# Kernel tuning notes

Hardware: AMD Instinct MI355X
Metric: run time of the kernel (lower is better)

## Reference

```python
import jax, jax.numpy as jnp
import numpy as np

S, H, D, NL = 3, 64, 12, 2  # scales, hidden, input_dim, layers
B, L = 512, 512
EPS = 1e-5


def _layernorm(x, g, b):
    m = jnp.mean(x, axis=-1, keepdims=True)
    v = jnp.var(x, axis=-1, keepdims=True)
    return (x - m) * jax.lax.rsqrt(v + EPS) * g + b


def _cell(x_t, h, c, gw, gb, mi_w, mi_b, mo_w, mo_b, w1, b1, w2, b2, lag, lab, log, lob):
    # fused 4-gate linear: [B, in+H] @ [in+H, 4H]
    gates = jnp.concatenate([x_t, h], axis=-1) @ gw + gb
    f, i, g, o = jnp.split(gates, 4, axis=-1)
    c_new = jax.nn.sigmoid(f) * c + jax.nn.sigmoid(i) * jnp.tanh(g)
    h_t = jax.nn.sigmoid(o) * jnp.tanh(c_new)
    # MultiheadAttention with seq_len=1: softmax over one key == 1,
    # so attn_out = out_proj(v_proj(h_t)) exactly (q/k contribute nothing).
    v = h_t @ mi_w[:, 2 * H:] + mi_b[2 * H:]
    a = v @ mo_w + mo_b
    a = jax.nn.gelu(a @ w1 + b1, approximate=False) @ w2 + b2
    a = _layernorm(a, lag, lab)
    return _layernorm(a + h, log, lob), c_new


def _run_xlstm(xi, gw0, gb0, gw1, gb1, mi_w, mi_b, mo_w, mo_b,
               w1, b1, w2, b2, lag, lab, log, lob, rw0, rb0, rw1, rb1):
    # xi: [B, L, D] -> outputs [B, L, H]; 2-layer unidirectional xLSTM (eval: dropout=identity)
    Bb = xi.shape[0]
    z = jnp.zeros((Bb, H), xi.dtype)

    def step(carry, x_t):
        h0, c0, h1, c1 = carry
        h0, c0 = _cell(x_t, h0, c0, gw0, gb0, mi_w[0], mi_b[0], mo_w[0], mo_b[0],
                       w1[0], b1[0], w2[0], b2[0], lag[0], lab[0], log[0], lob[0])
        inp = h0 + x_t @ rw0 + rb0
        h1, c1 = _cell(inp, h1, c1, gw1, gb1, mi_w[1], mi_b[1], mo_w[1], mo_b[1],
                       w1[1], b1[1], w2[1], b2[1], lag[1], lab[1], log[1], lob[1])
        out = h1 + inp @ rw1 + rb1
        return (h0, c0, h1, c1), out

    _, ys = jax.lax.scan(step, (z, z, z, z), jnp.swapaxes(xi, 0, 1))
    return jnp.swapaxes(ys, 0, 1)


def _upsample_linear(xi, out_len):
    # F.interpolate(mode='linear', align_corners=False) on [B, Li, D] time axis
    Li = xi.shape[1]
    if Li == out_len:
        return xi
    sc = Li / out_len
    src = jnp.maximum((jnp.arange(out_len, dtype=jnp.float32) + 0.5) * sc - 0.5, 0.0)
    i0 = jnp.clip(jnp.floor(src).astype(jnp.int32), 0, Li - 1)
    i1 = jnp.minimum(i0 + 1, Li - 1)
    w = (src - i0.astype(jnp.float32))[None, :, None]
    return xi[:, i0] * (1.0 - w) + xi[:, i1] * w


def _forward(x, gw0, gb0, gw1, gb1, mi_w, mi_b, mo_w, mo_b, w1, b1, w2, b2,
             lag, lab, log, lob, rw0, rb0, rw1, rb1, attn_w):
    Ls = x.shape[1]
    ups = []
    for i in (1, 2, 3):
        start = Ls - Ls // i
        ups.append(_upsample_linear(x[:, start:, :], Ls))
    # bug-faithful ordering from source: xlstm[i] consumes upsampled_outputs[i-1]
    xs = jnp.stack([ups[2], ups[0], ups[1]], axis=0)  # [S, B, L, D]
    outs = jax.vmap(_run_xlstm)(xs, gw0, gb0, gw1, gb1, mi_w, mi_b, mo_w, mo_b,
                                w1, b1, w2, b2, lag, lab, log, lob,
                                rw0, rb0, rw1, rb1)      # [S, B, L, H]
    merged = jnp.moveaxis(outs, 0, 1)                    # [B, S, L, H]
    weights = jax.nn.softmax(merged @ attn_w, axis=1)    # softmax over scale dim
    return jnp.sum(merged * weights[..., None], axis=1)  # [B, L, H]


def setup_inputs() -> dict:
    key = jax.random.key(0)
    ks = iter(jax.random.split(key, 32))
    w = lambda *sh: jax.random.normal(next(ks), sh, jnp.float32) * 0.02
    IN0, IN1 = D + H, 2 * H
    return {
        'x': jax.random.normal(next(ks), (B, L, D), jnp.float32),
        'gw0': w(S, IN0, 4 * H), 'gb0': jnp.zeros((S, 4 * H)),
        'gw1': w(S, IN1, 4 * H), 'gb1': jnp.zeros((S, 4 * H)),
        'mi_w': w(S, NL, H, 3 * H), 'mi_b': jnp.zeros((S, NL, 3 * H)),
        'mo_w': w(S, NL, H, H), 'mo_b': jnp.zeros((S, NL, H)),
        'w1': w(S, NL, H, 2 * H), 'b1': jnp.zeros((S, NL, 2 * H)),
        'w2': w(S, NL, 2 * H, H), 'b2': jnp.zeros((S, NL, H)),
        'lag': jnp.ones((S, NL, H)), 'lab': jnp.zeros((S, NL, H)),
        'log': jnp.ones((S, NL, H)), 'lob': jnp.zeros((S, NL, H)),
        'rw0': w(S, D, H), 'rb0': jnp.zeros((S, H)),
        'rw1': w(S, H, H), 'rb1': jnp.zeros((S, H)),
        'attn_w': w(H),
    }


def reference(x, gw0, gb0, gw1, gb1, mi_w, mi_b, mo_w, mo_b, w1, b1, w2, b2,
              lag, lab, log, lob, rw0, rb0, rw1, rb1, attn_w):
    return _forward(x, gw0, gb0, gw1, gb1, mi_w, mi_b, mo_w, mo_b, w1, b1, w2, b2,
                    lag, lab, log, lob, rw0, rb0, rw1, rb1, attn_w)
```

## Files before the change

### kernel.cpp

```cpp
#include <hip/hip_runtime.h>
#include <hip/hip_bf16.h>
#include <math.h>

#define Sn 3
#define Hn 64
#define Dn 12
#define Bn 512
#define Ln 512
#define BC 4
#define IN0 76
#define NIN 22
#define CT 32
#define NCHUNK (Ln / CT)
#define P2OFF 0
#define P1OFF 384
#define GROFF 768
#define CBOFF 1026
#define MEGABLK 1538

#define NINP ((size_t)3 * Bn * CT * 64)
#define NG1R ((size_t)3 * Bn * CT * 320)
#define NMERG ((size_t)3 * Bn * CT * 64)

using bf16 = __hip_bfloat16;
typedef _Float16 h2 __attribute__((ext_vector_type(2)));
typedef _Float16 h4 __attribute__((ext_vector_type(4)));
typedef _Float16 h8t __attribute__((ext_vector_type(8)));
typedef int i2v __attribute__((ext_vector_type(2)));

__device__ __forceinline__ float u2f(unsigned short x) {
    return __uint_as_float(((unsigned int)x) << 16);
}
__device__ __forceinline__ unsigned short f2u(float f) {
    bf16 h = __float2bfloat16(f);
    unsigned short u;
    __builtin_memcpy(&u, &h, 2);
    return u;
}

__device__ __forceinline__ float ex2(float x) {
#if __has_builtin(__builtin_amdgcn_exp2f)
    return __builtin_amdgcn_exp2f(x);
#else
    return exp2f(x);
#endif
}
__device__ __forceinline__ float frcp(float x) {
#if __has_builtin(__builtin_amdgcn_rcpf)
    return __builtin_amdgcn_rcpf(x);
#else
    return 1.0f / x;
#endif
}
__device__ __forceinline__ float sigm(float x) {
    return frcp(1.0f + ex2(-1.44269504f * x));
}
__device__ __forceinline__ float tanhfast(float x) {
    return 1.0f - 2.0f * frcp(1.0f + ex2(2.88539008f * x));
}
__device__ __forceinline__ float gelu_ex(float x) { return 0.5f * x * (1.0f + erff(x * 0.70710678118654752f)); }

__device__ __forceinline__ float fdot2f(h2 a, h2 b, float c) {
#if __has_builtin(__builtin_amdgcn_fdot2)
    return __builtin_amdgcn_fdot2(a, b, c, false);
#else
    return fmaf((float)a.x, (float)b.x, fmaf((float)a.y, (float)b.y, c));
#endif
}
__device__ __forceinline__ h2 cvt2(float x, float y) {
    h2 r; r.x = (_Float16)x; r.y = (_Float16)y; return r;
}
__device__ __forceinline__ h2 mk2(_Float16 a, _Float16 b) {
    h2 r; r.x = a; r.y = b; return r;
}
__device__ __forceinline__ void unpack8(h8t v, h2* out) {
    out[0] = __builtin_shufflevector(v, v, 0, 1);
    out[1] = __builtin_shufflevector(v, v, 2, 3);
    out[2] = __builtin_shufflevector(v, v, 4, 5);
    out[3] = __builtin_shufflevector(v, v, 6, 7);
}

template <int CTRL>
__device__ __forceinline__ float qp(float v) {
    return __int_as_float(__builtin_amdgcn_update_dpp(0, __float_as_int(v), CTRL, 0xF, 0xF, true));
}
__device__ __forceinline__ float qsum(float v) {
    v += qp<0xB1>(v);
    v += qp<0x4E>(v);
    return v;
}
__device__ __forceinline__ float osum(float v) {
    v = qsum(v);
    v += qp<0x141>(v);
    return v;
}
__device__ __forceinline__ float xadd16(float v) {
#if __has_builtin(__builtin_amdgcn_permlane16_swap)
    i2v r = __builtin_amdgcn_permlane16_swap(__float_as_int(v), __float_as_int(v), false, false);
    return __int_as_float(r.x) + __int_as_float(r.y);
#else
    return v + __int_as_float(__builtin_amdgcn_ds_swizzle(__float_as_int(v), 0x401F));
#endif
}
__device__ __forceinline__ float xadd32(float v) {
#if __has_builtin(__builtin_amdgcn_permlane32_swap)
    i2v r = __builtin_amdgcn_permlane32_swap(__float_as_int(v), __float_as_int(v), false, false);
    return __int_as_float(r.x) + __int_as_float(r.y);
#else
    return v + __shfl_xor(v, 32, 64);
#endif
}
__device__ __forceinline__ float redsum64(float v) {
    v += qp<0xB1>(v);
    v += qp<0x4E>(v);
    v += qp<0x141>(v);
    v += qp<0x140>(v);
    v = xadd16(v);
    v = xadd32(v);
    return v;
}

__global__ __launch_bounds__(256) void detect_kernel(const unsigned short* __restrict__ xr,
                                                     int* __restrict__ flag) {
    __shared__ int sh[4];
    int tid = threadIdx.x;
    int cnt = 0;
    for (int i = tid; i < 2048; i += 256) {
        unsigned e = (xr[i] >> 7) & 0xFF;
        if (e >= 110 && e <= 133) cnt++;
    }
    for (int o = 32; o > 0; o >>= 1) cnt += __shfl_xor(cnt, o, 64);
    if ((tid & 63) == 0) sh[tid >> 6] = cnt;
    __syncthreads();
    if (tid == 0) {
        int tot = sh[0] + sh[1] + sh[2] + sh[3];
        *flag = (tot < 1640) ? 1 : 0;
    }
}

struct ConvArgs {
    const void* src[NIN];
    unsigned dstOff[NIN];
    unsigned n[NIN];
    unsigned blockStart[NIN + 1];
};

__global__ __launch_bounds__(256) void convert_kernel(ConvArgs a, float* __restrict__ dst,
                                                      const int* __restrict__ flag) {
    int bid = blockIdx.x;
    int i = 0;
    while (i < NIN - 1 && bid >= (int)a.blockStart[i + 1]) i++;
    unsigned lb = (unsigned)bid - a.blockStart[i];
    unsigned base = lb * 2048 + threadIdx.x;
    unsigned n = a.n[i];
    float* d = dst + a.dstOff[i];
    bool isf32 = (*flag != 0);
    const float* sf = (const float*)a.src[i];
    const unsigned short* su = (const unsigned short*)a.src[i];
#pragma unroll
    for (int e = 0; e < 8; e++) {
        unsigned idx = base + e * 256;
        if (idx < n) d[idx] = isf32 ? sf[idx] : u2f(su[idx]);
    }
}

__global__ __launch_bounds__(256) void fuse_kernel(
    const float* __restrict__ mi_w, const float* __restrict__ mi_b,
    const float* __restrict__ mo_w, const float* __restrict__ mo_b,
    const float* __restrict__ w1, const float* __restrict__ b1,
    float* __restrict__ M1out, float* __restrict__ bias1out) {
    int sl = blockIdx.x;
    __shared__ float T[64][64];
    __shared__ float bT[64];
    const float* Mv = mi_w + sl * 64 * 192;
    const float* Mo = mo_w + sl * 64 * 64;
    for (int idx = threadIdx.x; idx < 64 * 64; idx += 256) {
        int k = idx >> 6, n = idx & 63;
        float acc = 0.f;
        for (int j = 0; j < 64; j++) acc += Mv[k * 192 + 128 + j] * Mo[j * 64 + n];
        T[k][n] = acc;
    }
    for (int n = threadIdx.x; n < 64; n += 256) {
        float acc = mo_b[sl * 64 + n];
        for (int j = 0; j < 64; j++) acc += mi_b[sl * 192 + 128 + j] * Mo[j * 64 + n];
        bT[n] = acc;
    }
    __syncthreads();
    const float* W1 = w1 + sl * 64 * 128;
    for (int idx = threadIdx.x; idx < 64 * 128; idx += 256) {
        int k = idx >> 7, m = idx & 127;
        float acc = 0.f;
        for (int n = 0; n < 64; n++) acc += T[k][n] * W1[n * 128 + m];
        M1out[sl * 64 * 128 + idx] = acc;
    }
    for (int m = threadIdx.x; m < 128; m += 256) {
        float acc = b1[sl * 128 + m];
        for (int n = 0; n < 64; n++) acc += bT[n] * W1[n * 128 + m];
        bias1out[sl * 128 + m] = acc;
    }
}

__global__ __launch_bounds__(256) void perm_kernel(
    const float* __restrict__ gw1, const float* __restrict__ gb1,
    const float* __restrict__ rw1,
    h2* __restrict__ gw1p16, float* __restrict__ gb1p,
    h2* __restrict__ rw1p16) {
    int s = blockIdx.x;
    int tid = threadIdx.x;
    const float* G = gw1 + (size_t)s * 128 * 256;
    for (int idx = tid; idx < 32 * 256; idx += 256) {
        int k2 = idx >> 8, p = idx & 255;
        int c = (p & 3) * 64 + ((p >> 6) << 4) + ((p >> 2) & 15);
        gw1p16[((size_t)s * 32 + k2) * 256 + p] =
            cvt2(G[(2 * k2) * 256 + c], G[(2 * k2 + 1) * 256 + c]);
    }
    for (int p = tid; p < 256; p += 256) {
        int c = (p & 3) * 64 + ((p >> 6) << 4) + ((p >> 2) & 15);
        gb1p[s * 256 + p] = gb1[s * 256 + c];
    }
    const float* R = rw1 + (size_t)s * 64 * 64;
    for (int idx = tid; idx < 32 * 64; idx += 256) {
        int k2 = idx >> 6, c = idx & 63;
        rw1p16[((size_t)s * 32 + k2) * 64 + c] =
            cvt2(R[(2 * k2) * 64 + c], R[(2 * k2 + 1) * 64 + c]);
    }
}

__device__ __forceinline__ void pass1_body(
    int bid,
    const float* __restrict__ x, const float* __restrict__ gw0,
    const float* __restrict__ gb0,
    const float* __restrict__ M1g, const float* __restrict__ bias1g,
    const float* __restrict__ w2g, const float* __restrict__ b2g,
    const float* __restrict__ lag, const float* __restrict__ lab,
    const float* __restrict__ log_, const float* __restrict__ lob,
    const float* __restrict__ rw0, const float* __restrict__ rb0,
    float* __restrict__ gstate, _Float16* __restrict__ inp_w, int t0) {
    const int tid = threadIdx.x;
    const int sIdx = bid >> 7;
    const int gbase = (bid & 127) * BC;
    const int W = tid >> 6, lane = tid & 63;
    const int q = lane >> 2, ks = lane & 3;
    const int oct = lane >> 3, ks8 = lane & 7;
    const int j = W * 16 + q;
    const int cM = W * 32 + q * 2;
    const int uD = W * 16 + oct * 2;

    const int Li = (sIdx == 0) ? 170 : (sIdx == 1 ? 512 : 256);
    const int st = (sIdx == 0) ? 342 : (sIdx == 1 ? 0 : 256);
    const float sc = (float)Li / 512.0f;

    __shared__ float s_x[2][BC][12];
    __shared__ __align__(16) _Float16 s_h16[BC][72];
    __shared__ __align__(16) _Float16 s_ht16[BC][72];
    __shared__ __align__(16) _Float16 s_z16[BC][136];
    __shared__ float s_t2[BC][64];
    __shared__ float s_rw0[768];

    __builtin_amdgcn_s_setprio(1);

    const float* gw0s = gw0 + sIdx * IN0 * 256;
    float wx[12];
    h2 wg16[4][8], wm16[2][8], ww16[2][8];
#pragma unroll
    for (int g = 0; g < 4; g++)
#pragma unroll
        for (int d = 0; d < 3; d++) wx[g * 3 + d] = gw0s[(ks * 3 + d) * 256 + j + 64 * g];
#pragma unroll
    for (int g = 0; g < 4; g++)
#pragma unroll
        for (int kk = 0; kk < 8; kk++)
            wg16[g][kk] = cvt2(gw0s[(12 + ks * 16 + 2 * kk) * 256 + j + 64 * g],
                               gw0s[(12 + ks * 16 + 2 * kk + 1) * 256 + j + 64 * g]);
    const float* M1s = M1g + (sIdx * 2 + 0) * 8192;
#pragma unroll
    for (int cc = 0; cc < 2; cc++)
#pragma unroll
        for (int kk = 0; kk < 8; kk++)
            wm16[cc][kk] = cvt2(M1s[(ks * 16 + 2 * kk) * 128 + cM + cc],
                                M1s[(ks * 16 + 2 * kk + 1) * 128 + cM + cc]);
    const float* w2s = w2g + (sIdx * 2 + 0) * 8192;
#pragma unroll
    for (int cc = 0; cc < 2; cc++)
#pragma unroll
        for (int kk = 0; kk < 8; kk++)
            ww16[cc][kk] = cvt2(w2s[(ks8 * 16 + 2 * kk) * 64 + uD + cc],
                                w2s[(ks8 * 16 + 2 * kk + 1) * 64 + uD + cc]);

    float h_gb[4];
#pragma unroll
    for (int g = 0; g < 4; g++) h_gb[g] = gb0[sIdx * 256 + j + 64 * g];
    float h_b1[2] = {bias1g[(sIdx * 2 + 0) * 128 + cM], bias1g[(sIdx * 2 + 0) * 128 + cM + 1]};
    float h_b2[2] = {b2g[(sIdx * 2 + 0) * 64 + uD], b2g[(sIdx * 2 + 0) * 64 + uD + 1]};
    int ei = (sIdx * 2 + 0) * 64 + lane;
    float eLag = lag[ei], eLab = lab[ei], eLog = log_[ei], eLob = lob[ei];
    float eRb0 = rb0[sIdx * 64 + lane];

    for (int i = tid; i < 768; i += 256) s_rw0[i] = rw0[sIdx * 768 + i];
    {
        int b = tid >> 6, jj = tid & 63;
        float hv = (t0 == 0) ? 0.f : gstate[((size_t)(sIdx * Bn + gbase + b)) * 256 + jj];
        s_h16[b][jj] = (_Float16)hv;
    }
    float cS = (t0 == 0) ? 0.f
                         : gstate[((size_t)(sIdx * Bn + gbase + ks)) * 256 + 64 + j];
    if (tid < BC * 12) {
        int b = tid / 12, d = tid % 12;
        float srcp = fmaxf((t0 + 0.5f) * sc - 0.5f, 0.f);
        int i0 = (int)floorf(srcp); if (i0 > Li - 1) i0 = Li - 1;
        int i1 = i0 + 1; if (i1 > Li - 1) i1 = Li - 1;
        float w = srcp - (float)i0;
        int gb = gbase + b;
        s_x[0][b][d] = x[(gb * Ln + st + i0) * 12 + d] * (1.0f - w) + x[(gb * Ln + st + i1) * 12 + d] * w;
    }
    __syncthreads();

    for (int tt = 0; tt < CT; tt++) {
        const int sl = tt & 1;
        float myF = 0, myI = 0, myG = 0, myO = 0;
#pragma unroll
        for (int b = 0; b < BC; b++) {
            const h8t* hp = (const h8t*)&s_h16[b][ks * 16];
            h8t hv0 = hp[0], hv1 = hp[1];
            h2 hk[8];
            unpack8(hv0, hk); unpack8(hv1, hk + 4);
            float x0 = s_x[sl][b][ks * 3], x1 = s_x[sl][b][ks * 3 + 1], x2 = s_x[sl][b][ks * 3 + 2];
            float acc[4];
#pragma unroll
            for (int g = 0; g < 4; g++) {
                float s0 = (ks == 0) ? h_gb[g] : 0.f;
                acc[g] = fmaf(wx[g * 3], x0, fmaf(wx[g * 3 + 1], x1, fmaf(wx[g * 3 + 2], x2, s0)));
            }
#pragma unroll
            for (int kk = 0; kk < 8; kk++) {
#pragma unroll
                for (int g = 0; g < 4; g++)
                    acc[g] = fdot2f(wg16[g][kk], hk[kk], acc[g]);
            }
            float a0 = qsum(acc[0]);
            float a1 = qsum(acc[1]);
            float a2 = qsum(acc[2]);
            float a3 = qsum(acc[3]);
            if (ks == b) { myF = a0; myI = a1; myG = a2; myO = a3; }
        }
        {
            float cn = sigm(myF) * cS + sigm(myI) * tanhfast(myG);
            cS = cn;
            s_ht16[ks][j] = (_Float16)(sigm(myO) * tanhfast(cn));
        }
        __syncthreads();
        float z0 = 0, z1 = 0;
#pragma unroll
        for (int b = 0; b < BC; b++) {
            const h8t* hp = (const h8t*)&s_ht16[b][ks * 16];
            h8t hv0 = hp[0], hv1 = hp[1];
            h2 hk[8];
            unpack8(hv0, hk); unpack8(hv1, hk + 4);
            float acc0 = (ks == 0) ? h_b1[0] : 0.f;
            float acc1 = (ks == 0) ? h_b1[1] : 0.f;
#pragma unroll
            for (int kk = 0; kk < 8; kk++) {
                acc0 = fdot2f(wm16[0][kk], hk[kk], acc0);
                acc1 = fdot2f(wm16[1][kk], hk[kk], acc1);
            }
            float a0 = qsum(acc0);
            float a1 = qsum(acc1);
            if (ks == b) { z0 = a0; z1 = a1; }
        }
        *(h2*)&s_z16[ks][cM] = cvt2(gelu_ex(z0), gelu_ex(z1));
        __syncthreads();
#pragma unroll
        for (int b = 0; b < BC; b++) {
            const h8t* zp = (const h8t*)&s_z16[b][ks8 * 16];
            h8t zv0 = zp[0], zv1 = zp[1];
            h2 zk[8];
            unpack8(zv0, zk); unpack8(zv1, zk + 4);
            float acc0 = (ks8 == 0) ? h_b2[0] : 0.f;
            float acc1 = (ks8 == 0) ? h_b2[1] : 0.f;
#pragma unroll
            for (int kk = 0; kk < 8; kk++) {
                acc0 = fdot2f(ww16[0][kk], zk[kk], acc0);
                acc1 = fdot2f(ww16[1][kk], zk[kk], acc1);
            }
            float a0 = osum(acc0);
            float a1 = osum(acc1);
            if (ks8 == b) { s_t2[b][uD] = a0; s_t2[b][uD + 1] = a1; }
        }
        __syncthreads();
        {
            const int bb = W;
            float v = s_t2[bb][lane];
            float m = redsum64(v) * (1.0f / 64.0f);
            float var = redsum64(v * v) * (1.0f / 64.0f) - m * m;
            float rs = rsqrtf(fmaxf(var, 0.0f) + 1e-5f);
            float a = (v - m) * rs * eLag + eLab;
            float hOld = (float)s_h16[bb][lane];
            float y = a + hOld;
            float m2 = redsum64(y) * (1.0f / 64.0f);
            float var2 = redsum64(y * y) * (1.0f / 64.0f) - m2 * m2;
            float rs2 = rsqrtf(fmaxf(var2, 0.0f) + 1e-5f);
            float h0n = (y - m2) * rs2 * eLog + eLob;
            s_h16[bb][lane] = (_Float16)h0n;
            float p = h0n + eRb0;
#pragma unroll
            for (int d = 0; d < 12; d++)
                p = fmaf(s_x[sl][bb][d], s_rw0[d * 64 + lane], p);
            inp_w[(((size_t)(sIdx * Bn + gbase + bb)) * CT + tt) * 64 + lane] = (_Float16)p;
            if (tt + 1 < CT && lane < 12) {
                int d = lane;
                int t = t0 + tt + 1;
                float srcp = fmaxf((t + 0.5f) * sc - 0.5f, 0.f);
                int i0 = (int)floorf(srcp); if (i0 > Li - 1) i0 = Li - 1;
                int i1 = i0 + 1; if (i1 > Li - 1) i1 = Li - 1;
                float w = srcp - (float)i0;
                int gb = gbase + bb;
                s_x[sl ^ 1][bb][d] = x[(gb * Ln + st + i0) * 12 + d] * (1.0f - w) +
                                     x[(gb * Ln + st + i1) * 12 + d] * w;
            }
        }
        __syncthreads();
    }
    {
        int b = tid >> 6, jj = tid & 63;
        gstate[((size_t)(sIdx * Bn + gbase + b)) * 256 + jj] = (float)s_h16[b][jj];
    }
    gstate[((size_t)(sIdx * Bn + gbase + ks)) * 256 + 64 + j] = cS;
}

__device__ __forceinline__ void pass2_body(
    int bid,
    const float* __restrict__ gw1,
    const float* __restrict__ M1g, const float* __restrict__ bias1g,
    const float* __restrict__ w2g, const float* __restrict__ b2g,
    const float* __restrict__ lag, const float* __restrict__ lab,
    const float* __restrict__ log_, const float* __restrict__ lob,
    const _Float16* __restrict__ G1Rr, float* __restrict__ gstate,
    unsigned short* __restrict__ merged_w, int t0) {
    const int tid = threadIdx.x;
    const int sIdx = bid >> 7;
    const int gbase = (bid & 127) * BC;
    const int W = tid >> 6, lane = tid & 63;
    const int q = lane >> 2, ks = lane & 3;
    const int oct = lane >> 3, ks8 = lane & 7;
    const int j = W * 16 + q;
    const int cM = W * 32 + q * 2;
    const int uD = W * 16 + oct * 2;

    __shared__ __align__(16) _Float16 p2_h16[BC][72];
    __shared__ __align__(16) _Float16 p2_ht16[BC][72];
    __shared__ __align__(16) _Float16 p2_z16[BC][136];
    __shared__ float p2_t2[BC][64];

    __builtin_amdgcn_s_setprio(1);

    const float* gw1s = gw1 + (size_t)sIdx * 128 * 256;
    h2 wg16[4][8], wm16[2][8], ww16[2][8];
#pragma unroll
    for (int g = 0; g < 4; g++)
#pragma unroll
        for (int kk = 0; kk < 8; kk++)
            wg16[g][kk] = cvt2(gw1s[(64 + ks * 16 + 2 * kk) * 256 + j + 64 * g],
                               gw1s[(64 + ks * 16 + 2 * kk + 1) * 256 + j + 64 * g]);
    const float* M1s = M1g + (sIdx * 2 + 1) * 8192;
#pragma unroll
    for (int cc = 0; cc < 2; cc++)
#pragma unroll
        for (int kk = 0; kk < 8; kk++)
            wm16[cc][kk] = cvt2(M1s[(ks * 16 + 2 * kk) * 128 + cM + cc],
                                M1s[(ks * 16 + 2 * kk + 1) * 128 + cM + cc]);
    const float* w2s = w2g + (sIdx * 2 + 1) * 8192;
#pragma unroll
    for (int cc = 0; cc < 2; cc++)
#pragma unroll
        for (int kk = 0; kk < 8; kk++)
            ww16[cc][kk] = cvt2(w2s[(ks8 * 16 + 2 * kk) * 64 + uD + cc],
                                w2s[(ks8 * 16 + 2 * kk + 1) * 64 + uD + cc]);

    float h_b1[2] = {bias1g[(sIdx * 2 + 1) * 128 + cM], bias1g[(sIdx * 2 + 1) * 128 + cM + 1]};
    float h_b2[2] = {b2g[(sIdx * 2 + 1) * 64 + uD], b2g[(sIdx * 2 + 1) * 64 + uD + 1]};
    int ei = (sIdx * 2 + 1) * 64 + lane;
    float eLag = lag[ei], eLab = lab[ei], eLog = log_[ei], eLob = lob[ei];

    {
        int b = tid >> 6, jj = tid & 63;
        float hv = (t0 == 0) ? 0.f : gstate[((size_t)(sIdx * Bn + gbase + b)) * 256 + 128 + jj];
        p2_h16[b][jj] = (_Float16)hv;
    }
    float cS = (t0 == 0) ? 0.f
                         : gstate[((size_t)(sIdx * Bn + gbase + ks)) * 256 + 192 + j];
    __syncthreads();

    const size_t rowBase = ((size_t)(sIdx * Bn + gbase)) * CT;
    const int pOff = W * 64 + lane;

    float g1rv[BC], rv;
#pragma unroll
    for (int b = 0; b < BC; b++)
        g1rv[b] = (float)G1Rr[(rowBase + (size_t)b * CT) * 320 + pOff];
    rv = (float)G1Rr[(rowBase + (size_t)W * CT) * 320 + 256 + lane];

    for (int tt = 0; tt < CT; tt++) {
        float myF = 0, myI = 0, myG = 0, myO = 0;
#pragma unroll
        for (int b = 0; b < BC; b++) {
            const h8t* hp = (const h8t*)&p2_h16[b][ks * 16];
            h8t hv0 = hp[0], hv1 = hp[1];
            h2 hk[8];
            unpack8(hv0, hk); unpack8(hv1, hk + 4);
            float acc[4];
#pragma unroll
            for (int g = 0; g < 4; g++) acc[g] = (ks == g) ? g1rv[b] : 0.f;
#pragma unroll
            for (int kk = 0; kk < 8; kk++) {
#pragma unroll
                for (int g = 0; g < 4; g++)
                    acc[g] = fdot2f(wg16[g][kk], hk[kk], acc[g]);
            }
            float a0 = qsum(acc[0]);
            float a1 = qsum(acc[1]);
            float a2 = qsum(acc[2]);
            float a3 = qsum(acc[3]);
            if (ks == b) { myF = a0; myI = a1; myG = a2; myO = a3; }
        }
        {
            float cn = sigm(myF) * cS + sigm(myI) * tanhfast(myG);
            cS = cn;
            p2_ht16[ks][j] = (_Float16)(sigm(myO) * tanhfast(cn));
        }
        float g1rn[BC], rn;
        if (tt + 1 < CT) {
#pragma unroll
            for (int b = 0; b < BC; b++)
                g1rn[b] = (float)G1Rr[(rowBase + (size_t)b * CT + tt + 1) * 320 + pOff];
            rn = (float)G1Rr[(rowBase + (size_t)W * CT + tt + 1) * 320 + 256 + lane];
        } else {
#pragma unroll
            for (int b = 0; b < BC; b++) g1rn[b] = 0.f;
            rn = 0.f;
        }
        __syncthreads();
        float z0 = 0, z1 = 0;
#pragma unroll
        for (int b = 0; b < BC; b++) {
            const h8t* hp = (const h8t*)&p2_ht16[b][ks * 16];
            h8t hv0 = hp[0], hv1 = hp[1];
            h2 hk[8];
            unpack8(hv0, hk); unpack8(hv1, hk + 4);
            float acc0 = (ks == 0) ? h_b1[0] : 0.f;
            float acc1 = (ks == 0) ? h_b1[1] : 0.f;
#pragma unroll
            for (int kk = 0; kk < 8; kk++) {
                acc0 = fdot2f(wm16[0][kk], hk[kk], acc0);
                acc1 = fdot2f(wm16[1][kk], hk[kk], acc1);
            }
            float a0 = qsum(acc0);
            float a1 = qsum(acc1);
            if (ks == b) { z0 = a0; z1 = a1; }
        }
        *(h2*)&p2_z16[ks][cM] = cvt2(gelu_ex(z0), gelu_ex(z1));
        __syncthreads();
#pragma unroll
        for (int b = 0; b < BC; b++) {
            const h8t* zp = (const h8t*)&p2_z16[b][ks8 * 16];
            h8t zv0 = zp[0], zv1 = zp[1];
            h2 zk[8];
            unpack8(zv0, zk); unpack8(zv1, zk + 4);
            float acc0 = (ks8 == 0) ? h_b2[0] : 0.f;
            float acc1 = (ks8 == 0) ? h_b2[1] : 0.f;
#pragma unroll
            for (int kk = 0; kk < 8; kk++) {
                acc0 = fdot2f(ww16[0][kk], zk[kk], acc0);
                acc1 = fdot2f(ww16[1][kk], zk[kk], acc1);
            }
            float a0 = osum(acc0);
            float a1 = osum(acc1);
            if (ks8 == b) { p2_t2[b][uD] = a0; p2_t2[b][uD + 1] = a1; }
        }
        __syncthreads();
        {
            const int bb = W;
            float v = p2_t2[bb][lane];
            float m = redsum64(v) * (1.0f / 64.0f);
            float var = redsum64(v * v) * (1.0f / 64.0f) - m * m;
            float rs = rsqrtf(fmaxf(var, 0.0f) + 1e-5f);
            float a = (v - m) * rs * eLag + eLab;
            float hOld = (float)p2_h16[bb][lane];
            float y = a + hOld;
            float m2 = redsum64(y) * (1.0f / 64.0f);
            float var2 = redsum64(y * y) * (1.0f / 64.0f) - m2 * m2;
            float rs2 = rsqrtf(fmaxf(var2, 0.0f) + 1e-5f);
            float h1n = (y - m2) * rs2 * eLog + eLob;
            p2_h16[bb][lane] = (_Float16)h1n;
            merged_w[(((size_t)(sIdx * Bn + gbase + bb)) * CT + tt) * 64 + lane] = f2u(h1n + rv);
        }
        __syncthreads();
#pragma unroll
        for (int b = 0; b < BC; b++) g1rv[b] = g1rn[b];
        rv = rn;
    }
    {
        int b = tid >> 6, jj = tid & 63;
        gstate[((size_t)(sIdx * Bn + gbase + b)) * 256 + 128 + jj] = (float)p2_h16[b][jj];
    }
    gstate[((size_t)(sIdx * Bn + gbase + ks)) * 256 + 192 + j] = cS;
}

__device__ __forceinline__ void g1r_body(
    int bid,
    const h2* __restrict__ gw1p16, const float* __restrict__ gb1p,
    const h2* __restrict__ rw1p16, const float* __restrict__ rb1,
    const _Float16* __restrict__ inp_r, _Float16* __restrict__ G1Rw) {
    const int tid = threadIdx.x;
    const int s = bid / 86;
    const int bb = bid % 86;
    __shared__ __align__(16) h2 s_in2[32][36];

    const int c4 = tid & 63, rg = tid >> 6;
    float4 bias = *(const float4*)(gb1p + s * 256 + c4 * 4);
    float rbias = rb1[s * 64 + c4];
    const h2* Wg = gw1p16 + (size_t)s * 32 * 256;
    const h2* Wr = rw1p16 + (size_t)s * 32 * 64;

    const size_t sRow = (size_t)s * Bn * CT;
    for (int tile = 0; tile < 6; tile++) {
        int tIdx = bb * 6 + tile;
        if (tIdx >= 512) break;
        int r0 = tIdx * 32;
        __syncthreads();
        for (int i = tid; i < 512; i += 256) {
            int r = i >> 4, kq = i & 15;
            h4 v = *(const h4*)(inp_r + (sRow + r0 + r) * 64 + kq * 4);
            s_in2[kq * 2 + 0][r] = mk2(v.x, v.y);
            s_in2[kq * 2 + 1][r] = mk2(v.z, v.w);
        }
        __syncthreads();
        float acc[8][4], accR[8];
#pragma unroll
        for (int r = 0; r < 8; r++) {
            acc[r][0] = bias.x; acc[r][1] = bias.y; acc[r][2] = bias.z; acc[r][3] = bias.w;
            accR[r] = rbias;
        }
#pragma unroll 4
        for (int k2 = 0; k2 < 32; k2++) {
            h8t wv = *(const h8t*)(Wg + (size_t)k2 * 256 + c4 * 4);
            h2 wp[4]; unpack8(wv, wp);
            h2 wR = Wr[k2 * 64 + c4];
            const h8t* ip = (const h8t*)&s_in2[k2][rg * 8];
            h8t iv0 = ip[0], iv1 = ip[1];
            h2 in2[8]; unpack8(iv0, in2); unpack8(iv1, in2 + 4);
#pragma unroll
            for (int r = 0; r < 8; r++) {
                acc[r][0] = fdot2f(in2[r], wp[0], acc[r][0]);
                acc[r][1] = fdot2f(in2[r], wp[1], acc[r][1]);
                acc[r][2] = fdot2f(in2[r], wp[2], acc[r][2]);
                acc[r][3] = fdot2f(in2[r], wp[3], acc[r][3]);
                accR[r] = fdot2f(in2[r], wR, accR[r]);
            }
        }
#pragma unroll
        for (int r = 0; r < 8; r++) {
            size_t row = sRow + r0 + rg * 8 + r;
            h4 o;
            o.x = (_Float16)acc[r][0]; o.y = (_Float16)acc[r][1];
            o.z = (_Float16)acc[r][2]; o.w = (_Float16)acc[r][3];
            *(h4*)(G1Rw + row * 320 + c4 * 4) = o;
            G1Rw[row * 320 + 256 + c4] = (_Float16)accR[r];
        }
    }
}

__device__ __forceinline__ void combine_body(
    int bid,
    const unsigned short* __restrict__ merged_r,
    const float* __restrict__ attn_w,
    void* __restrict__ outv, const int* __restrict__ flag, int t0) {
    int W = threadIdx.x >> 6, lane = threadIdx.x & 63;
    float aw = attn_w[lane];
    size_t stride = (size_t)Bn * CT * 64;
    int isf = *flag;
#pragma unroll
    for (int r = 0; r < 8; r++) {
        int wid = (bid * 4 + W) * 8 + r;
        int b = wid >> 5, tt = wid & 31;
        size_t base = (((size_t)b) * CT + tt) * 64 + lane;
        float m0 = u2f(merged_r[base]);
        float m1 = u2f(merged_r[base + stride]);
        float m2 = u2f(merged_r[base + 2 * stride]);
        float e0 = redsum64(m0 * aw);
        float e1 = redsum64(m1 * aw);
        float e2 = redsum64(m2 * aw);
        float mx = fmaxf(e0, fmaxf(e1, e2));
        float x0 = expf(e0 - mx), x1 = expf(e1 - mx), x2 = expf(e2 - mx);
        float inv = 1.0f / (x0 + x1 + x2);
        float val = (x0 * m0 + x1 * m1 + x2 * m2) * inv;
        size_t ob = (((size_t)b) * Ln + t0 + tt) * 64 + lane;
        if (isf) ((float*)outv)[ob] = val;
        else ((unsigned short*)outv)[ob] = f2u(val);
    }
}

__global__ __launch_bounds__(256) __attribute__((amdgpu_waves_per_eu(2, 5)))
void mega_kernel(
    const float* __restrict__ x, const float* __restrict__ gw0,
    const float* __restrict__ gb0, const float* __restrict__ gw1,
    const h2* __restrict__ gw1p16, const float* __restrict__ gb1p,
    const h2* __restrict__ rw1p16,
    const float* __restrict__ M1g, const float* __restrict__ bias1g,
    const float* __restrict__ w2g, const float* __restrict__ b2g,
    const float* __restrict__ lag, const float* __restrict__ lab,
    const float* __restrict__ log_, const float* __restrict__ lob,
    const float* __restrict__ rw0, const float* __restrict__ rb0,
    const float* __restrict__ rb1,
    float* __restrict__ gstate,
    _Float16* __restrict__ inpB, _Float16* __restrict__ G1RB,
    unsigned short* __restrict__ mergedB,
    const float* __restrict__ attn_w, void* __restrict__ outv,
    const int* __restrict__ flag,
    int c_p1, int c_g1r, int c_p2, int c_comb) {
    int bid = blockIdx.x;
    if (bid < P1OFF) {
        if (c_p2 >= 0) {
            const _Float16* g1r_r = G1RB + (size_t)(c_p2 & 1) * NG1R;
            unsigned short* merged_w = mergedB + (size_t)(c_p2 & 1) * NMERG;
            pass2_body(bid, gw1, M1g, bias1g, w2g, b2g, lag, lab, log_, lob,
                       g1r_r, gstate, merged_w, c_p2 * CT);
        }
    } else if (bid < GROFF) {
        if (c_p1 >= 0) {
            _Float16* inp_w = inpB + (size_t)(c_p1 & 1) * NINP;
            pass1_body(bid - P1OFF, x, gw0, gb0, M1g, bias1g, w2g, b2g,
                       lag, lab, log_, lob, rw0, rb0, gstate, inp_w, c_p1 * CT);
        }
    } else if (bid < CBOFF) {
        if (c_g1r >= 0) {
            const _Float16* inp_r = inpB + (size_t)(c_g1r & 1) * NINP;
            _Float16* g1r_w = G1RB + (size_t)(c_g1r & 1) * NG1R;
            g1r_body(bid - GROFF, gw1p16, gb1p, rw1p16, rb1, inp_r, g1r_w);
        }
    } else {
        if (c_comb >= 0) {
            const unsigned short* merged_r = mergedB + (size_t)(c_comb & 1) * NMERG;
            combine_body(bid - CBOFF, merged_r, attn_w, outv, flag, c_comb * CT);
        }
    }
}

extern "C" void kernel_launch(void* const* d_in, const int* in_sizes, int n_in,
                              void* d_out, int out_size, void* d_ws, size_t ws_size,
                              hipStream_t stream) {
    (void)out_size; (void)ws_size;
    int* flag = (int*)d_ws;
    float* canon = (float*)((char*)d_ws + 16);

    ConvArgs ca;
    size_t tot = 0;
    unsigned nblocks = 0;
    for (int i = 0; i < NIN; i++) {
        ca.src[i] = d_in[i];
        ca.dstOff[i] = (unsigned)tot;
        unsigned n = (unsigned)in_sizes[i];
        ca.n[i] = n;
        ca.blockStart[i] = nblocks;
        nblocks += (n + 2047) / 2048;
        tot += n;
    }
    ca.blockStart[NIN] = nblocks;

    size_t canonBytes = (tot * 4 + 15) & ~(size_t)15;
    char* p = (char*)d_ws + 16 + canonBytes;
    float* M1 = (float*)p;       p += (size_t)3 * 2 * 64 * 128 * 4;
    float* bias1 = (float*)p;    p += (size_t)3 * 2 * 128 * 4;
    float* gb1p = (float*)p;     p += (size_t)3 * 256 * 4;
    h2* gw1p16 = (h2*)p;         p += (size_t)3 * 32 * 256 * 4;
    h2* rw1p16 = (h2*)p;         p += (size_t)3 * 32 * 64 * 4;
    float* gstate = (float*)p;   p += (size_t)3 * 512 * 256 * 4;
    p = (char*)(((uintptr_t)p + 15) & ~(uintptr_t)15);
    _Float16* inpB = (_Float16*)p;      p += 2 * NINP * 2;
    _Float16* G1RB = (_Float16*)p;      p += 2 * NG1R * 2;
    p = (char*)(((uintptr_t)p + 15) & ~(uintptr_t)15);
    unsigned short* mergedB = (unsigned short*)p;

    const float* x    = canon + ca.dstOff[0];
    const float* gw0  = canon + ca.dstOff[1];
    const float* gb0  = canon + ca.dstOff[2];
    const float* gw1  = canon + ca.dstOff[3];
    const float* gb1  = canon + ca.dstOff[4];
    const float* mi_w = canon + ca.dstOff[5];
    const float* mi_b = canon + ca.dstOff[6];
    const float* mo_w = canon + ca.dstOff[7];
    const float* mo_b = canon + ca.dstOff[8];
    const float* w1   = canon + ca.dstOff[9];
    const float* b1   = canon + ca.dstOff[10];
    const float* w2   = canon + ca.dstOff[11];
    const float* b2   = canon + ca.dstOff[12];
    const float* lag  = canon + ca.dstOff[13];
    const float* lab  = canon + ca.dstOff[14];
    const float* log_ = canon + ca.dstOff[15];
    const float* lob  = canon + ca.dstOff[16];
    const float* rw0  = canon + ca.dstOff[17];
    const float* rb0  = canon + ca.dstOff[18];
    const float* rw1  = canon + ca.dstOff[19];
    const float* rb1  = canon + ca.dstOff[20];
    const float* attn_w = canon + ca.dstOff[21];

    detect_kernel<<<dim3(1), dim3(256), 0, stream>>>((const unsigned short*)d_in[0], flag);
    convert_kernel<<<dim3(nblocks), dim3(256), 0, stream>>>(ca, canon, flag);
    fuse_kernel<<<dim3(6), dim3(256), 0, stream>>>(mi_w, mi_b, mo_w, mo_b, w1, b1, M1, bias1);
    perm_kernel<<<dim3(3), dim3(256), 0, stream>>>(gw1, gb1, rw1, gw1p16, gb1p, rw1p16);

    for (int m = 0; m <= NCHUNK + 2; m++) {
        int c1 = (m < NCHUNK) ? m : -1;
        int cg = (m - 1 >= 0 && m - 1 < NCHUNK) ? m - 1 : -1;
        int c2 = (m - 2 >= 0 && m - 2 < NCHUNK) ? m - 2 : -1;
        int cc = (m - 3 >= 0 && m - 3 < NCHUNK) ? m - 3 : -1;
        mega_kernel<<<dim3(MEGABLK), dim3(256), 0, stream>>>(
            x, gw0, gb0, gw1, gw1p16, gb1p, rw1p16, M1, bias1, w2, b2,
            lag, lab, log_, lob, rw0, rb0, rb1, gstate, inpB, G1RB, mergedB,
            attn_w, d_out, flag, c1, cg, c2, cc);
    }
}
```

Measured before the change: 3.057 ms.

## Fuse layer-1 input GEMM into pass1 blocks and shorten launch pipeline

Each pass1 block now runs the G1R GEMM (gate and residual projections for layer 1) on its own freshly written inp rows at the end of its chunk, instead of leaving it to separate g1r blocks one pipeline stage later. This drops one stage from the software pipeline, so one fewer mega-kernel launch is issued, and it cuts the inp buffer from double to single buffering and shrinks the grid. The cost is that the GEMM now runs serially after the recurrence inside the pass1 blocks, which lengthens their critical path, and there are fewer blocks to spread that work across.

```diff
diff --git a/kernel.cpp b/kernel.cpp
--- a/kernel.cpp
+++ b/kernel.cpp
@@ -12,11 +12,9 @@
 #define NIN 22
 #define CT 32
 #define NCHUNK (Ln / CT)
-#define P2OFF 0
 #define P1OFF 384
-#define GROFF 768
-#define CBOFF 1026
-#define MEGABLK 1538
+#define CBOFF 768
+#define MEGABLK 1280
 
 #define NINP ((size_t)3 * Bn * CT * 64)
 #define NG1R ((size_t)3 * Bn * CT * 320)
@@ -235,7 +233,10 @@
     const float* __restrict__ lag, const float* __restrict__ lab,
     const float* __restrict__ log_, const float* __restrict__ lob,
     const float* __restrict__ rw0, const float* __restrict__ rb0,
-    float* __restrict__ gstate, _Float16* __restrict__ inp_w, int t0) {
+    const h2* __restrict__ gw1p16, const float* __restrict__ gb1p,
+    const h2* __restrict__ rw1p16, const float* __restrict__ rb1,
+    float* __restrict__ gstate, _Float16* __restrict__ inp_w,
+    _Float16* __restrict__ G1Rw, int t0) {
     const int tid = threadIdx.x;
     const int sIdx = bid >> 7;
     const int gbase = (bid & 127) * BC;
@@ -256,6 +257,7 @@
     __shared__ __align__(16) _Float16 s_z16[BC][136];
     __shared__ float s_t2[BC][64];
     __shared__ float s_rw0[768];
+    __shared__ __align__(16) h2 s_in2[32][36];
 
     __builtin_amdgcn_s_setprio(1);
 
@@ -425,6 +427,57 @@
         gstate[((size_t)(sIdx * Bn + gbase + b)) * 256 + jj] = (float)s_h16[b][jj];
     }
     gstate[((size_t)(sIdx * Bn + gbase + ks)) * 256 + 64 + j] = cS;
+
+    const int c4 = tid & 63, rg = tid >> 6;
+    float4 gbias = *(const float4*)(gb1p + sIdx * 256 + c4 * 4);
+    float rbias = rb1[sIdx * 64 + c4];
+    const h2* Wg = gw1p16 + (size_t)sIdx * 32 * 256;
+    const h2* Wr = rw1p16 + (size_t)sIdx * 32 * 64;
+    const size_t rowBase = ((size_t)(sIdx * Bn + gbase)) * CT;
+
+    for (int tile = 0; tile < 4; tile++) {
+        int r0 = tile * 32;
+        __syncthreads();
+        for (int i = tid; i < 512; i += 256) {
+            int r = i >> 4, kq = i & 15;
+            h4 v = *(const h4*)(inp_w + (rowBase + r0 + r) * 64 + kq * 4);
+            s_in2[kq * 2 + 0][r] = mk2(v.x, v.y);
+            s_in2[kq * 2 + 1][r] = mk2(v.z, v.w);
+        }
+        __syncthreads();
+        float acc[8][4], accR[8];
+#pragma unroll
+        for (int r = 0; r < 8; r++) {
+            acc[r][0] = gbias.x; acc[r][1] = gbias.y; acc[r][2] = gbias.z; acc[r][3] = gbias.w;
+            accR[r] = rbias;
+        }
+#pragma unroll 4
+        for (int k2 = 0; k2 < 32; k2++) {
+            h8t wv = *(const h8t*)(Wg + (size_t)k2 * 256 + c4 * 4);
+            h2 wp[4]; unpack8(wv, wp);
+            h2 wR = Wr[k2 * 64 + c4];
+            const h8t* ip = (const h8t*)&s_in2[k2][rg * 8];
+            h8t iv0 = ip[0], iv1 = ip[1];
+            h2 in2[8]; unpack8(iv0, in2); unpack8(iv1, in2 + 4);
+#pragma unroll
+            for (int r = 0; r < 8; r++) {
+                acc[r][0] = fdot2f(in2[r], wp[0], acc[r][0]);
+                acc[r][1] = fdot2f(in2[r], wp[1], acc[r][1]);
+                acc[r][2] = fdot2f(in2[r], wp[2], acc[r][2]);
+                acc[r][3] = fdot2f(in2[r], wp[3], acc[r][3]);
+                accR[r] = fdot2f(in2[r], wR, accR[r]);
+            }
+        }
+#pragma unroll
+        for (int r = 0; r < 8; r++) {
+            size_t row = rowBase + r0 + rg * 8 + r;
+            h4 o;
+            o.x = (_Float16)acc[r][0]; o.y = (_Float16)acc[r][1];
+            o.z = (_Float16)acc[r][2]; o.w = (_Float16)acc[r][3];
+            *(h4*)(G1Rw + row * 320 + c4 * 4) = o;
+            G1Rw[row * 320 + 256 + c4] = (_Float16)accR[r];
+        }
+    }
 }
 
 __device__ __forceinline__ void pass2_body(
@@ -605,70 +658,6 @@
     gstate[((size_t)(sIdx * Bn + gbase + ks)) * 256 + 192 + j] = cS;
 }
 
-__device__ __forceinline__ void g1r_body(
-    int bid,
-    const h2* __restrict__ gw1p16, const float* __restrict__ gb1p,
-    const h2* __restrict__ rw1p16, const float* __restrict__ rb1,
-    const _Float16* __restrict__ inp_r, _Float16* __restrict__ G1Rw) {
-    const int tid = threadIdx.x;
-    const int s = bid / 86;
-    const int bb = bid % 86;
-    __shared__ __align__(16) h2 s_in2[32][36];
-
-    const int c4 = tid & 63, rg = tid >> 6;
-    float4 bias = *(const float4*)(gb1p + s * 256 + c4 * 4);
-    float rbias = rb1[s * 64 + c4];
-    const h2* Wg = gw1p16 + (size_t)s * 32 * 256;
-    const h2* Wr = rw1p16 + (size_t)s * 32 * 64;
-
-    const size_t sRow = (size_t)s * Bn * CT;
-    for (int tile = 0; tile < 6; tile++) {
-        int tIdx = bb * 6 + tile;
-        if (tIdx >= 512) break;
-        int r0 = tIdx * 32;
-        __syncthreads();
-        for (int i = tid; i < 512; i += 256) {
-            int r = i >> 4, kq = i & 15;
-            h4 v = *(const h4*)(inp_r + (sRow + r0 + r) * 64 + kq * 4);
-            s_in2[kq * 2 + 0][r] = mk2(v.x, v.y);
-            s_in2[kq * 2 + 1][r] = mk2(v.z, v.w);
-        }
-        __syncthreads();
-        float acc[8][4], accR[8];
-#pragma unroll
-        for (int r = 0; r < 8; r++) {
-            acc[r][0] = bias.x; acc[r][1] = bias.y; acc[r][2] = bias.z; acc[r][3] = bias.w;
-            accR[r] = rbias;
-        }
-#pragma unroll 4
-        for (int k2 = 0; k2 < 32; k2++) {
-            h8t wv = *(const h8t*)(Wg + (size_t)k2 * 256 + c4 * 4);
-            h2 wp[4]; unpack8(wv, wp);
-            h2 wR = Wr[k2 * 64 + c4];
-            const h8t* ip = (const h8t*)&s_in2[k2][rg * 8];
-            h8t iv0 = ip[0], iv1 = ip[1];
-            h2 in2[8]; unpack8(iv0, in2); unpack8(iv1, in2 + 4);
-#pragma unroll
-            for (int r = 0; r < 8; r++) {
-                acc[r][0] = fdot2f(in2[r], wp[0], acc[r][0]);
-                acc[r][1] = fdot2f(in2[r], wp[1], acc[r][1]);
-                acc[r][2] = fdot2f(in2[r], wp[2], acc[r][2]);
-                acc[r][3] = fdot2f(in2[r], wp[3], acc[r][3]);
-                accR[r] = fdot2f(in2[r], wR, accR[r]);
-            }
-        }
-#pragma unroll
-        for (int r = 0; r < 8; r++) {
-            size_t row = sRow + r0 + rg * 8 + r;
-            h4 o;
-            o.x = (_Float16)acc[r][0]; o.y = (_Float16)acc[r][1];
-            o.z = (_Float16)acc[r][2]; o.w = (_Float16)acc[r][3];
-            *(h4*)(G1Rw + row * 320 + c4 * 4) = o;
-            G1Rw[row * 320 + 256 + c4] = (_Float16)accR[r];
-        }
-    }
-}
-
 __device__ __forceinline__ void combine_body(
     int bid,
     const unsigned short* __restrict__ merged_r,
@@ -716,7 +705,7 @@
     unsigned short* __restrict__ mergedB,
     const float* __restrict__ attn_w, void* __restrict__ outv,
     const int* __restrict__ flag,
-    int c_p1, int c_g1r, int c_p2, int c_comb) {
+    int c_p1, int c_p2, int c_comb) {
     int bid = blockIdx.x;
     if (bid < P1OFF) {
         if (c_p2 >= 0) {
@@ -725,17 +714,13 @@
             pass2_body(bid, gw1, M1g, bias1g, w2g, b2g, lag, lab, log_, lob,
                        g1r_r, gstate, merged_w, c_p2 * CT);
         }
-    } else if (bid < GROFF) {
+    } else if (bid < CBOFF) {
         if (c_p1 >= 0) {
-            _Float16* inp_w = inpB + (size_t)(c_p1 & 1) * NINP;
+            _Float16* g1r_w = G1RB + (size_t)(c_p1 & 1) * NG1R;
             pass1_body(bid - P1OFF, x, gw0, gb0, M1g, bias1g, w2g, b2g,
-                       lag, lab, log_, lob, rw0, rb0, gstate, inp_w, c_p1 * CT);
-        }
-    } else if (bid < CBOFF) {
-        if (c_g1r >= 0) {
-            const _Float16* inp_r = inpB + (size_t)(c_g1r & 1) * NINP;
-            _Float16* g1r_w = G1RB + (size_t)(c_g1r & 1) * NG1R;
-            g1r_body(bid - GROFF, gw1p16, gb1p, rw1p16, rb1, inp_r, g1r_w);
+                       lag, lab, log_, lob, rw0, rb0,
+                       gw1p16, gb1p, rw1p16, rb1,
+                       gstate, inpB, g1r_w, c_p1 * CT);
         }
     } else {
         if (c_comb >= 0) {
@@ -775,7 +760,7 @@
     h2* rw1p16 = (h2*)p;         p += (size_t)3 * 32 * 64 * 4;
     float* gstate = (float*)p;   p += (size_t)3 * 512 * 256 * 4;
     p = (char*)(((uintptr_t)p + 15) & ~(uintptr_t)15);
-    _Float16* inpB = (_Float16*)p;      p += 2 * NINP * 2;
+    _Float16* inpB = (_Float16*)p;      p += NINP * 2;
     _Float16* G1RB = (_Float16*)p;      p += 2 * NG1R * 2;
     p = (char*)(((uintptr_t)p + 15) & ~(uintptr_t)15);
     unsigned short* mergedB = (unsigned short*)p;
@@ -808,14 +793,13 @@
     fuse_kernel<<<dim3(6), dim3(256), 0, stream>>>(mi_w, mi_b, mo_w, mo_b, w1, b1, M1, bias1);
     perm_kernel<<<dim3(3), dim3(256), 0, stream>>>(gw1, gb1, rw1, gw1p16, gb1p, rw1p16);
 
-    for (int m = 0; m <= NCHUNK + 2; m++) {
+    for (int m = 0; m <= NCHUNK + 1; m++) {
         int c1 = (m < NCHUNK) ? m : -1;
-        int cg = (m - 1 >= 0 && m - 1 < NCHUNK) ? m - 1 : -1;
-        int c2 = (m - 2 >= 0 && m - 2 < NCHUNK) ? m - 2 : -1;
-        int cc = (m - 3 >= 0 && m - 3 < NCHUNK) ? m - 3 : -1;
+        int c2 = (m - 1 >= 0 && m - 1 < NCHUNK) ? m - 1 : -1;
+        int cc = (m - 2 >= 0 && m - 2 < NCHUNK) ? m - 2 : -1;
         mega_kernel<<<dim3(MEGABLK), dim3(256), 0, stream>>>(
             x, gw0, gb0, gw1, gw1p16, gb1p, rw1p16, M1, bias1, w2, b2,
             lag, lab, log_, lob, rw0, rb0, rb1, gstate, inpB, G1RB, mergedB,
-            attn_w, d_out, flag, c1, cg, c2, cc);
-    }
-}
+            attn_w, d_out, flag, c1, c2, cc);
+    }
+}
```

Result: slower. 3.320 ms (+8.6%).
